# Kernel tuning notes

Measured on AMD Instinct MI355X. Metric: run time of the kernel, lower is better.

The kernel has to match this reference:

```python
import jax, jax.numpy as jnp
import numpy as np

B, S, D, H = 4, 1024, 2048, 16
HD = D // H
SCALE = float(np.sqrt(HD))


def setup_inputs() -> dict:
    key = jax.random.key(0)
    ks = jax.random.split(key, 11)
    std = 1.0 / np.sqrt(D)
    inp = {
        'q': jax.random.normal(ks[0], (B, S, D), jnp.float32),
        'k': jax.random.normal(ks[1], (B, S, D), jnp.float32),
        'v': jax.random.normal(ks[2], (B, S, D), jnp.float32),
        'wq_w': jax.random.uniform(ks[3], (D, D), jnp.float32, -std, std),
        'wq_b': jax.random.uniform(ks[4], (D,), jnp.float32, -std, std),
        'wk_w': jax.random.uniform(ks[5], (D, D), jnp.float32, -std, std),
        'wk_b': jax.random.uniform(ks[6], (D,), jnp.float32, -std, std),
        'wv_w': jax.random.uniform(ks[7], (D, D), jnp.float32, -std, std),
        'wv_b': jax.random.uniform(ks[8], (D,), jnp.float32, -std, std),
        'wo_w': jax.random.uniform(ks[9], (D, D), jnp.float32, -std, std),
        'wo_b': jax.random.uniform(ks[10], (D,), jnp.float32, -std, std),
    }
    return inp


def reference(q, k, v, wq_w, wq_b, wk_w, wk_b, wv_w, wv_b, wo_w, wo_b):
    # Linear projections (torch Linear: x @ W.T + b), split into heads: [B,H,S,HD]
    Q = (q @ wq_w.T + wq_b).reshape(B, S, H, HD).transpose(0, 2, 1, 3)
    K = (k @ wk_w.T + wk_b).reshape(B, S, H, HD).transpose(0, 2, 1, 3)
    V = (v @ wv_w.T + wv_b).reshape(B, S, H, HD).transpose(0, 2, 1, 3)
    # scaled dot-product attention; mask=None, dropout identity (eval)
    scores = jnp.einsum('bhqd,bhkd->bhqk', Q, K) / SCALE  # [B,H,S,S]
    attn = jax.nn.softmax(scores, axis=-1)
    context = jnp.einsum('bhqk,bhkd->bhqd', attn, V)      # [B,H,S,HD]
    context = context.transpose(0, 2, 1, 3).reshape(B, S, D)
    output = context @ wo_w.T + wo_b
    return output, attn
```

## Files before the change

kernel.cpp:

```cpp
#include <hip/hip_runtime.h>
#include <hip/hip_bf16.h>


typedef __attribute__((ext_vector_type(4)))  float f32x4;
typedef __attribute__((ext_vector_type(16))) float f32x16;
typedef __attribute__((ext_vector_type(8))) short  bf16x8;
typedef __attribute__((ext_vector_type(4))) short  short4v;
typedef __attribute__((ext_vector_type(8))) short  short8v;

__device__ __forceinline__ short f2b(float f) {
  __hip_bfloat16 h = __float2bfloat16(f);
  return __builtin_bit_cast(short, h);
}
__device__ __forceinline__ float b2f(short s) {
  __hip_bfloat16 h = __builtin_bit_cast(__hip_bfloat16, s);
  return __bfloat162float(h);
}

__global__ void cast_all(
    const float* __restrict__ q,  const float* __restrict__ k,  const float* __restrict__ v,
    const float* __restrict__ w0, const float* __restrict__ w1, const float* __restrict__ w2,
    const float* __restrict__ w3,
    __hip_bfloat16* __restrict__ qd, __hip_bfloat16* __restrict__ kd, __hip_bfloat16* __restrict__ vd,
    __hip_bfloat16* __restrict__ d0, __hip_bfloat16* __restrict__ d1, __hip_bfloat16* __restrict__ d2,
    __hip_bfloat16* __restrict__ d3)
{
  const int c0 = blockIdx.x * blockDim.x + threadIdx.x;
#pragma unroll
  for (int it = 0; it < 10; ++it) {
    int c = c0 + it * 524288;
    const float* in; __hip_bfloat16* out; size_t off;
    if (c < 3145728) {
      int seg = c >> 20; off = (size_t)(c & 1048575) * 8;
      in  = seg == 0 ? q  : (seg == 1 ? k  : v);
      out = seg == 0 ? qd : (seg == 1 ? kd : vd);
    } else {
      int c2 = c - 3145728;
      int seg = c2 >> 19; off = (size_t)(c2 & 524287) * 8;
      in  = seg == 0 ? w0 : (seg == 1 ? w1 : (seg == 2 ? w2 : w3));
      out = seg == 0 ? d0 : (seg == 1 ? d1 : (seg == 2 ? d2 : d3));
    }
    float4 a = *(const float4*)(in + off);
    float4 b = *(const float4*)(in + off + 4);
    short8v o;
    o[0] = f2b(a.x); o[1] = f2b(a.y); o[2] = f2b(a.z); o[3] = f2b(a.w);
    o[4] = f2b(b.x); o[5] = f2b(b.y); o[6] = f2b(b.z); o[7] = f2b(b.w);
    *(short8v*)(out + off) = o;
  }
}

__device__ __forceinline__ void gload_lds16(const __hip_bfloat16* g, char* l) {
  __builtin_amdgcn_global_load_lds(
      (const __attribute__((address_space(1))) unsigned int*)g,
      (__attribute__((address_space(3))) unsigned int*)l, 16, 0, 0);
}

template<bool SWAP>
__device__ __forceinline__ void gemm_core(
    const __hip_bfloat16* ga0, const __hip_bfloat16* gb0,
    char* As, char* Bs, char* lA0, char* lB0,
    int wm, int wn, int l16, int g, f32x4 (&acc)[4][4])
{
#pragma unroll 1
  for (int kt = 0; kt < 64; ++kt) {
    __syncthreads();
    gload_lds16(ga0,             lA0);
    gload_lds16(ga0 + 16 * 2048, lA0 + 1024);
    gload_lds16(gb0,             lB0);
    gload_lds16(gb0 + 16 * 2048, lB0 + 1024);
    ga0 += 32; gb0 += 32;
    asm volatile("s_waitcnt vmcnt(0)" ::: "memory");
    __syncthreads();
    bf16x8 a[4], b[4];
#pragma unroll
    for (int mf = 0; mf < 4; ++mf)
      a[mf] = *(const bf16x8*)(As + (wm + mf * 16 + l16) * 64 + g * 16);
#pragma unroll
    for (int nf = 0; nf < 4; ++nf)
      b[nf] = *(const bf16x8*)(Bs + (wn + nf * 16 + l16) * 64 + g * 16);
#pragma unroll
    for (int mf = 0; mf < 4; ++mf)
#pragma unroll
      for (int nf = 0; nf < 4; ++nf) {
        if (SWAP)
          acc[mf][nf] = __builtin_amdgcn_mfma_f32_16x16x32_bf16(b[nf], a[mf], acc[mf][nf], 0, 0, 0);
        else
          acc[mf][nf] = __builtin_amdgcn_mfma_f32_16x16x32_bf16(a[mf], b[nf], acc[mf][nf], 0, 0, 0);
      }
  }
}

__global__ __launch_bounds__(256, 2) void gemm_qkv(
    const __hip_bfloat16* __restrict__ qbf, const __hip_bfloat16* __restrict__ kbf,
    const __hip_bfloat16* __restrict__ vbf,
    const __hip_bfloat16* __restrict__ wqb, const __hip_bfloat16* __restrict__ wkb,
    const __hip_bfloat16* __restrict__ wvb,
    const float* __restrict__ bq, const float* __restrict__ bk, const float* __restrict__ bv,
    __hip_bfloat16* __restrict__ Qh, __hip_bfloat16* __restrict__ Kh,
    __hip_bfloat16* __restrict__ Vt)
{
  __shared__ __align__(16) char smem[34816];
  char* As = smem;
  char* Bs = smem + 16384;

  const int z = blockIdx.z;
  const __hip_bfloat16* A  = z == 0 ? qbf : (z == 1 ? kbf : vbf);
  const __hip_bfloat16* Bt = z == 0 ? wqb : (z == 1 ? wkb : wvb);
  const float* bias        = z == 0 ? bq  : (z == 1 ? bk  : bv);
  __hip_bfloat16* C        = z == 0 ? Qh  : (z == 1 ? Kh  : Vt);

  const int tid  = threadIdx.x;
  const int lane = tid & 63, wid = tid >> 6;
  const int l16  = lane & 15, g = lane >> 4;
  const int m0 = blockIdx.y * 128, n0 = blockIdx.x * 128;
  const int wm = (wid >> 1) * 64, wn = (wid & 1) * 64;

  f32x4 acc[4][4];
#pragma unroll
  for (int i = 0; i < 4; ++i)
#pragma unroll
    for (int j = 0; j < 4; ++j) acc[i][j] = f32x4{0.f, 0.f, 0.f, 0.f};

  const __hip_bfloat16* ga0 = A  + (size_t)(m0 + wid * 32 + (lane >> 2)) * 2048 + (lane & 3) * 8;
  const __hip_bfloat16* gb0 = Bt + (size_t)(n0 + wid * 32 + (lane >> 2)) * 2048 + (lane & 3) * 8;
  char* lA0 = As + wid * 2048;
  char* lB0 = Bs + wid * 2048;

  if (z == 2) gemm_core<false>(ga0, gb0, As, Bs, lA0, lB0, wm, wn, l16, g, acc);
  else        gemm_core<true >(ga0, gb0, As, Bs, lA0, lB0, wm, wn, l16, g, acc);

  const int h = n0 >> 7, bb = m0 >> 10, sbase = m0 & 1023;
  const int c8 = (tid & 15) * 8;
  __syncthreads();
  char* Cs = smem;
  if (z != 2) {
#pragma unroll
    for (int nf = 0; nf < 4; ++nf) {
      f32x4 bvv = *(const f32x4*)(bias + n0 + wn + nf * 16 + g * 4);
#pragma unroll
      for (int mf = 0; mf < 4; ++mf) {
        int m  = wm + mf * 16 + l16;
        int nc = wn + nf * 16 + g * 4;
        short4v pk;
#pragma unroll
        for (int r = 0; r < 4; ++r) pk[r] = f2b(acc[mf][nf][r] + bvv[r]);
        *(short4v*)(Cs + m * 272 + nc * 2) = pk;
      }
    }
    __syncthreads();
#pragma unroll
    for (int p = 0; p < 8; ++p) {
      int row = p * 16 + (tid >> 4);
      bf16x8 val = *(const bf16x8*)(Cs + row * 272 + c8 * 2);
      *(bf16x8*)(C + (((size_t)bb * 16 + h) * 1024 + sbase + row) * 128 + c8) = val;
    }
  } else {
#pragma unroll
    for (int nf = 0; nf < 4; ++nf) {
      float bvv = bias[n0 + wn + nf * 16 + l16];
#pragma unroll
      for (int mf = 0; mf < 4; ++mf) {
        int hd = wn + nf * 16 + l16;
        int s0 = wm + mf * 16 + g * 4;
        short4v pk;
#pragma unroll
        for (int r = 0; r < 4; ++r) pk[r] = f2b(acc[mf][nf][r] + bvv);
        *(short4v*)(Cs + hd * 272 + s0 * 2) = pk;
      }
    }
    __syncthreads();
#pragma unroll
    for (int p = 0; p < 8; ++p) {
      int hd = p * 16 + (tid >> 4);
      bf16x8 val = *(const bf16x8*)(Cs + hd * 272 + c8 * 2);
      *(bf16x8*)(C + (((size_t)bb * 16 + h) * 128 + hd) * 1024 + sbase + c8) = val;
    }
  }
}

__global__ __launch_bounds__(256, 2) void gemm_out(
    const __hip_bfloat16* __restrict__ A, const __hip_bfloat16* __restrict__ Bt,
    const float* __restrict__ bias, float* __restrict__ C)
{
  __shared__ __align__(16) char smem[32768];
  char* As = smem;
  char* Bs = smem + 16384;
  const int tid  = threadIdx.x;
  const int lane = tid & 63, wid = tid >> 6;
  const int l16  = lane & 15, g = lane >> 4;
  const int m0 = blockIdx.y * 128, n0 = blockIdx.x * 128;
  const int wm = (wid >> 1) * 64, wn = (wid & 1) * 64;

  f32x4 acc[4][4];
#pragma unroll
  for (int i = 0; i < 4; ++i)
#pragma unroll
    for (int j = 0; j < 4; ++j) acc[i][j] = f32x4{0.f, 0.f, 0.f, 0.f};

  const __hip_bfloat16* ga0 = A  + (size_t)(m0 + wid * 32 + (lane >> 2)) * 2048 + (lane & 3) * 8;
  const __hip_bfloat16* gb0 = Bt + (size_t)(n0 + wid * 32 + (lane >> 2)) * 2048 + (lane & 3) * 8;
  char* lA0 = As + wid * 2048;
  char* lB0 = Bs + wid * 2048;

  gemm_core<true>(ga0, gb0, As, Bs, lA0, lB0, wm, wn, l16, g, acc);

#pragma unroll
  for (int nf = 0; nf < 4; ++nf) {
    f32x4 bv = *(const f32x4*)(bias + n0 + wn + nf * 16 + g * 4);
#pragma unroll
    for (int mf = 0; mf < 4; ++mf) {
      int m = m0 + wm + mf * 16 + l16;
      int n = n0 + wn + nf * 16 + g * 4;
      f32x4 o;
#pragma unroll
      for (int r = 0; r < 4; ++r) o[r] = acc[mf][nf][r] + bv[r];
      *(f32x4*)(C + (size_t)m * 2048 + n) = o;
    }
  }
}

__global__ __launch_bounds__(512, 4) void attn_kernel(
    const __hip_bfloat16* __restrict__ Qh,
    const __hip_bfloat16* __restrict__ Kh,
    const __hip_bfloat16* __restrict__ Vt,
    float* __restrict__ attn,
    __hip_bfloat16* __restrict__ ctx)
{
  __shared__ __align__(16) char Plds[32 * 2048];
  __shared__ float red[8 * 32];
  __shared__ float invs[32];

  const int tid = threadIdx.x, lane = tid & 63, w = tid >> 6;
  const int l16 = lane & 15, g = lane >> 4;
  const int l31 = lane & 31, kh = lane >> 5;

  const int bid = blockIdx.x;
  const int xcd = bid & 7, j = bid >> 3;
  const int bh  = xcd * 8 + (j >> 5);
  const int q0  = (j & 31) << 5;

  const __hip_bfloat16* Qp = Qh + ((size_t)bh * 1024 + q0) * 128;
  const __hip_bfloat16* Kp = Kh + (size_t)bh * 1024 * 128;
  const __hip_bfloat16* Vp = Vt + (size_t)bh * 128 * 1024;
  float* ap = attn + ((size_t)bh * 1024 + q0) * 1024;

  bf16x8 qb[8];
#pragma unroll
  for (int s = 0; s < 8; ++s)
    qb[s] = *(const bf16x8*)(Qp + (size_t)l31 * 128 + s * 16 + kh * 8);

  const float esc = 0.08838834764831845f;
  float rs = 0.f;

#pragma unroll
  for (int pass = 0; pass < 4; ++pass) {
    const int keybase = pass * 256 + w * 32;
    const __hip_bfloat16* kr = Kp + (size_t)(keybase + l31) * 128 + kh * 8;
    bf16x8 kb[8];
#pragma unroll
    for (int s = 0; s < 8; ++s) kb[s] = *(const bf16x8*)(kr + s * 16);
    f32x16 acc;
#pragma unroll
    for (int i = 0; i < 16; ++i) acc[i] = 0.f;
    __builtin_amdgcn_s_setprio(1);
#pragma unroll
    for (int s = 0; s < 8; ++s)
      acc = __builtin_amdgcn_mfma_f32_32x32x16_bf16(kb[s], qb[s], acc, 0, 0, 0);
    __builtin_amdgcn_s_setprio(0);
#pragma unroll
    for (int grp = 0; grp < 4; ++grp) {
      short4v pk;
#pragma unroll
      for (int jj = 0; jj < 4; ++jj) {
        float e = __expf(acc[grp * 4 + jj] * esc);
        rs += e;
        pk[jj] = f2b(e);
      }
      int key0 = keybase + grp * 8 + kh * 4;
      *(short4v*)(Plds + l31 * 2048 + ((key0 * 2) ^ ((l31 & 7) << 4))) = pk;
    }
  }
  rs += __shfl_xor(rs, 32, 64);
  if (lane < 32) red[w * 32 + l31] = rs;
  __syncthreads();
  if (tid < 32) {
    float t = 0.f;
#pragma unroll
    for (int ww = 0; ww < 8; ++ww) t += red[ww * 32 + tid];
    invs[tid] = 1.0f / t;
  }

  f32x4 acc2[2];
  acc2[0] = f32x4{0.f, 0.f, 0.f, 0.f};
  acc2[1] = f32x4{0.f, 0.f, 0.f, 0.f};
  {
    const char* pr0 = Plds + l16 * 2048;
    const char* pr1 = Plds + (16 + l16) * 2048;
    const int sw = (l16 & 7) << 4;
#pragma unroll 4
    for (int kt = 0; kt < 32; ++kt) {
      int cb = (kt * 64 + g * 16) ^ sw;
      bf16x8 pa0 = *(const bf16x8*)(pr0 + cb);
      bf16x8 pa1 = *(const bf16x8*)(pr1 + cb);
      const __hip_bfloat16* vr = Vp + (size_t)(16 * w + l16) * 1024 + kt * 32 + g * 8;
      bf16x8 vb = *(const bf16x8*)vr;
      __builtin_amdgcn_s_setprio(1);
      acc2[0] = __builtin_amdgcn_mfma_f32_16x16x32_bf16(pa0, vb, acc2[0], 0, 0, 0);
      acc2[1] = __builtin_amdgcn_mfma_f32_16x16x32_bf16(pa1, vb, acc2[1], 0, 0, 0);
      __builtin_amdgcn_s_setprio(0);
    }
  }
  __syncthreads();

  {
    const int row = 4 * w + g;
    const float invr = invs[row];
    const char* rp = Plds + row * 2048;
    const int sw = (row & 7) << 4;
    float* apr = ap + (size_t)row * 1024;
#pragma unroll
    for (int it = 0; it < 16; ++it) {
      int col = it * 64 + l16 * 4;
      short4v pb = *(const short4v*)(rp + ((col * 2) ^ sw));
      f32x4 val;
#pragma unroll
      for (int r = 0; r < 4; ++r) val[r] = b2f(pb[r]) * invr;
      __builtin_nontemporal_store(val, (f32x4*)(apr + col));
    }
  }
  __syncthreads();

  {
    __hip_bfloat16* cs = (__hip_bfloat16*)Plds;
#pragma unroll
    for (int t = 0; t < 2; ++t) {
      f32x4 iv = *(const f32x4*)(invs + t * 16 + g * 4);
#pragma unroll
      for (int r = 0; r < 4; ++r)
        cs[(t * 16 + g * 4 + r) * 128 + 16 * w + l16] = __float2bfloat16(acc2[t][r] * iv[r]);
    }
    __syncthreads();
    const int row = tid >> 4, c8 = (tid & 15) * 8;
    bf16x8 val = *(const bf16x8*)(cs + row * 128 + c8);
    const int bb = bh >> 4, h = bh & 15;
    *(bf16x8*)(ctx + ((size_t)(bb * 1024 + q0 + row)) * 2048 + h * 128 + c8) = val;
  }
}

extern "C" void kernel_launch(void* const* d_in, const int* in_sizes, int n_in,
                              void* d_out, int out_size, void* d_ws, size_t ws_size,
                              hipStream_t stream) {
  const float* q    = (const float*)d_in[0];
  const float* k    = (const float*)d_in[1];
  const float* v    = (const float*)d_in[2];
  const float* wq_w = (const float*)d_in[3];
  const float* wq_b = (const float*)d_in[4];
  const float* wk_w = (const float*)d_in[5];
  const float* wk_b = (const float*)d_in[6];
  const float* wv_w = (const float*)d_in[7];
  const float* wv_b = (const float*)d_in[8];
  const float* wo_w = (const float*)d_in[9];
  const float* wo_b = (const float*)d_in[10];

  const size_t BSD = (size_t)4 * 1024 * 2048;
  const size_t DD  = (size_t)2048 * 2048;

  float* out  = (float*)d_out;
  float* attn = out + BSD;

  __hip_bfloat16* qbf = (__hip_bfloat16*)attn;
  __hip_bfloat16* kbf = qbf + BSD;
  __hip_bfloat16* vbf = kbf + BSD;

  __hip_bfloat16* wqb = (__hip_bfloat16*)d_ws;
  __hip_bfloat16* wkb = wqb + DD;
  __hip_bfloat16* wvb = wkb + DD;
  __hip_bfloat16* wob = wvb + DD;
  __hip_bfloat16* Qh  = wob + DD;
  __hip_bfloat16* Kh  = Qh + BSD;
  __hip_bfloat16* Vt  = Kh + BSD;
  __hip_bfloat16* ctx = Vt + BSD;

  cast_all<<<2048, 256, 0, stream>>>(q, k, v, wq_w, wk_w, wv_w, wo_w,
                                     qbf, kbf, vbf, wqb, wkb, wvb, wob);

  gemm_qkv<<<dim3(16, 32, 3), dim3(256), 0, stream>>>(
      qbf, kbf, vbf, wqb, wkb, wvb, wq_b, wk_b, wv_b, Qh, Kh, Vt);

  attn_kernel<<<dim3(2048), dim3(512), 0, stream>>>(Qh, Kh, Vt, attn, ctx);

  gemm_out<<<dim3(16, 32), dim3(256), 0, stream>>>(ctx, wob, wo_b, out);
}
```

Baseline: 372.3 us.

## Double GEMM K-step to 64 with XOR-swizzled LDS and raise occupancy

```diff
diff --git a/kernel.cpp b/kernel.cpp
--- a/kernel.cpp
+++ b/kernel.cpp
@@ -56,41 +56,51 @@
 }
 
 template<bool SWAP>
-__device__ __forceinline__ void gemm_core(
+__device__ __forceinline__ void gemm_core64(
     const __hip_bfloat16* ga0, const __hip_bfloat16* gb0,
     char* As, char* Bs, char* lA0, char* lB0,
     int wm, int wn, int l16, int g, f32x4 (&acc)[4][4])
 {
+  const int sw = (l16 & 7) << 4;
 #pragma unroll 1
-  for (int kt = 0; kt < 64; ++kt) {
+  for (int kt = 0; kt < 32; ++kt) {
     __syncthreads();
-    gload_lds16(ga0,             lA0);
-    gload_lds16(ga0 + 16 * 2048, lA0 + 1024);
-    gload_lds16(gb0,             lB0);
-    gload_lds16(gb0 + 16 * 2048, lB0 + 1024);
-    ga0 += 32; gb0 += 32;
+#pragma unroll
+    for (int c = 0; c < 4; ++c) {
+      gload_lds16(ga0 + c * 16384, lA0 + c * 1024);
+      gload_lds16(gb0 + c * 16384, lB0 + c * 1024);
+    }
+    ga0 += 64; gb0 += 64;
     asm volatile("s_waitcnt vmcnt(0)" ::: "memory");
     __syncthreads();
-    bf16x8 a[4], b[4];
-#pragma unroll
-    for (int mf = 0; mf < 4; ++mf)
-      a[mf] = *(const bf16x8*)(As + (wm + mf * 16 + l16) * 64 + g * 16);
-#pragma unroll
-    for (int nf = 0; nf < 4; ++nf)
-      b[nf] = *(const bf16x8*)(Bs + (wn + nf * 16 + l16) * 64 + g * 16);
-#pragma unroll
-    for (int mf = 0; mf < 4; ++mf)
+#pragma unroll
+    for (int ks = 0; ks < 2; ++ks) {
+      bf16x8 a[4];
+#pragma unroll
+      for (int mf = 0; mf < 4; ++mf)
+        a[mf] = *(const bf16x8*)(As + (wm + mf * 16 + l16) * 128 + ((ks * 64 + g * 16) ^ sw));
 #pragma unroll
       for (int nf = 0; nf < 4; ++nf) {
-        if (SWAP)
-          acc[mf][nf] = __builtin_amdgcn_mfma_f32_16x16x32_bf16(b[nf], a[mf], acc[mf][nf], 0, 0, 0);
-        else
-          acc[mf][nf] = __builtin_amdgcn_mfma_f32_16x16x32_bf16(a[mf], b[nf], acc[mf][nf], 0, 0, 0);
-      }
-  }
-}
-
-__global__ __launch_bounds__(256, 2) void gemm_qkv(
+        bf16x8 b = *(const bf16x8*)(Bs + (wn + nf * 16 + l16) * 128 + ((ks * 64 + g * 16) ^ sw));
+#pragma unroll
+        for (int mf = 0; mf < 4; ++mf) {
+          if (SWAP)
+            acc[mf][nf] = __builtin_amdgcn_mfma_f32_16x16x32_bf16(b, a[mf], acc[mf][nf], 0, 0, 0);
+          else
+            acc[mf][nf] = __builtin_amdgcn_mfma_f32_16x16x32_bf16(a[mf], b, acc[mf][nf], 0, 0, 0);
+        }
+      }
+    }
+  }
+}
+
+__device__ __forceinline__ const __hip_bfloat16* stage_src(
+    const __hip_bfloat16* M, int base, int wid, int lane) {
+  return M + (size_t)(base + wid * 32 + (lane >> 3)) * 2048
+           + (((lane & 7) ^ ((lane >> 3) & 7)) * 8);
+}
+
+__global__ __launch_bounds__(256, 3) void gemm_qkv(
     const __hip_bfloat16* __restrict__ qbf, const __hip_bfloat16* __restrict__ kbf,
     const __hip_bfloat16* __restrict__ vbf,
     const __hip_bfloat16* __restrict__ wqb, const __hip_bfloat16* __restrict__ wkb,
@@ -99,7 +109,7 @@
     __hip_bfloat16* __restrict__ Qh, __hip_bfloat16* __restrict__ Kh,
     __hip_bfloat16* __restrict__ Vt)
 {
-  __shared__ __align__(16) char smem[34816];
+  __shared__ __align__(16) char smem[32768];
   char* As = smem;
   char* Bs = smem + 16384;
 
@@ -121,64 +131,75 @@
 #pragma unroll
     for (int j = 0; j < 4; ++j) acc[i][j] = f32x4{0.f, 0.f, 0.f, 0.f};
 
-  const __hip_bfloat16* ga0 = A  + (size_t)(m0 + wid * 32 + (lane >> 2)) * 2048 + (lane & 3) * 8;
-  const __hip_bfloat16* gb0 = Bt + (size_t)(n0 + wid * 32 + (lane >> 2)) * 2048 + (lane & 3) * 8;
-  char* lA0 = As + wid * 2048;
-  char* lB0 = Bs + wid * 2048;
-
-  if (z == 2) gemm_core<false>(ga0, gb0, As, Bs, lA0, lB0, wm, wn, l16, g, acc);
-  else        gemm_core<true >(ga0, gb0, As, Bs, lA0, lB0, wm, wn, l16, g, acc);
-
-  const int h = n0 >> 7, bb = m0 >> 10, sbase = m0 & 1023;
+  const __hip_bfloat16* ga0 = stage_src(A,  m0, wid, lane);
+  const __hip_bfloat16* gb0 = stage_src(Bt, n0, wid, lane);
+  char* lA0 = As + wid * 4096;
+  char* lB0 = Bs + wid * 4096;
+
+  if (z == 2) gemm_core64<false>(ga0, gb0, As, Bs, lA0, lB0, wm, wn, l16, g, acc);
+  else        gemm_core64<true >(ga0, gb0, As, Bs, lA0, lB0, wm, wn, l16, g, acc);
+
+  const int hh = n0 >> 7, bb = m0 >> 10, sbase = m0 & 1023;
   const int c8 = (tid & 15) * 8;
-  __syncthreads();
   char* Cs = smem;
   if (z != 2) {
 #pragma unroll
-    for (int nf = 0; nf < 4; ++nf) {
-      f32x4 bvv = *(const f32x4*)(bias + n0 + wn + nf * 16 + g * 4);
-#pragma unroll
-      for (int mf = 0; mf < 4; ++mf) {
-        int m  = wm + mf * 16 + l16;
-        int nc = wn + nf * 16 + g * 4;
-        short4v pk;
-#pragma unroll
-        for (int r = 0; r < 4; ++r) pk[r] = f2b(acc[mf][nf][r] + bvv[r]);
-        *(short4v*)(Cs + m * 272 + nc * 2) = pk;
-      }
-    }
-    __syncthreads();
-#pragma unroll
-    for (int p = 0; p < 8; ++p) {
-      int row = p * 16 + (tid >> 4);
-      bf16x8 val = *(const bf16x8*)(Cs + row * 272 + c8 * 2);
-      *(bf16x8*)(C + (((size_t)bb * 16 + h) * 1024 + sbase + row) * 128 + c8) = val;
+    for (int h = 0; h < 2; ++h) {
+      __syncthreads();
+      if ((wid >> 1) == h) {
+#pragma unroll
+        for (int nf = 0; nf < 4; ++nf) {
+          f32x4 bvv = *(const f32x4*)(bias + n0 + wn + nf * 16 + g * 4);
+#pragma unroll
+          for (int mf = 0; mf < 4; ++mf) {
+            int sl = mf * 16 + l16;
+            int hd = wn + nf * 16 + g * 4;
+            short4v pk;
+#pragma unroll
+            for (int r = 0; r < 4; ++r) pk[r] = f2b(acc[mf][nf][r] + bvv[r]);
+            *(short4v*)(Cs + sl * 272 + hd * 2) = pk;
+          }
+        }
+      }
+      __syncthreads();
+#pragma unroll
+      for (int p = 0; p < 4; ++p) {
+        int rl = p * 16 + (tid >> 4);
+        bf16x8 val = *(const bf16x8*)(Cs + rl * 272 + c8 * 2);
+        *(bf16x8*)(C + (((size_t)bb * 16 + hh) * 1024 + sbase + h * 64 + rl) * 128 + c8) = val;
+      }
     }
   } else {
 #pragma unroll
-    for (int nf = 0; nf < 4; ++nf) {
-      float bvv = bias[n0 + wn + nf * 16 + l16];
-#pragma unroll
-      for (int mf = 0; mf < 4; ++mf) {
-        int hd = wn + nf * 16 + l16;
-        int s0 = wm + mf * 16 + g * 4;
-        short4v pk;
-#pragma unroll
-        for (int r = 0; r < 4; ++r) pk[r] = f2b(acc[mf][nf][r] + bvv);
-        *(short4v*)(Cs + hd * 272 + s0 * 2) = pk;
-      }
-    }
-    __syncthreads();
-#pragma unroll
-    for (int p = 0; p < 8; ++p) {
-      int hd = p * 16 + (tid >> 4);
-      bf16x8 val = *(const bf16x8*)(Cs + hd * 272 + c8 * 2);
-      *(bf16x8*)(C + (((size_t)bb * 16 + h) * 128 + hd) * 1024 + sbase + c8) = val;
-    }
-  }
-}
-
-__global__ __launch_bounds__(256, 2) void gemm_out(
+    for (int h = 0; h < 2; ++h) {
+      __syncthreads();
+      if ((wid & 1) == h) {
+#pragma unroll
+        for (int nf = 0; nf < 4; ++nf) {
+          float bvv = bias[n0 + wn + nf * 16 + l16];
+#pragma unroll
+          for (int mf = 0; mf < 4; ++mf) {
+            int hdl = nf * 16 + l16;
+            int s0  = wm + mf * 16 + g * 4;
+            short4v pk;
+#pragma unroll
+            for (int r = 0; r < 4; ++r) pk[r] = f2b(acc[mf][nf][r] + bvv);
+            *(short4v*)(Cs + hdl * 272 + s0 * 2) = pk;
+          }
+        }
+      }
+      __syncthreads();
+#pragma unroll
+      for (int p = 0; p < 4; ++p) {
+        int rl = p * 16 + (tid >> 4);
+        bf16x8 val = *(const bf16x8*)(Cs + rl * 272 + c8 * 2);
+        *(bf16x8*)(C + (((size_t)bb * 16 + hh) * 128 + h * 64 + rl) * 1024 + sbase + c8) = val;
+      }
+    }
+  }
+}
+
+__global__ __launch_bounds__(256, 3) void gemm_out(
     const __hip_bfloat16* __restrict__ A, const __hip_bfloat16* __restrict__ Bt,
     const float* __restrict__ bias, float* __restrict__ C)
 {
@@ -197,12 +218,12 @@
 #pragma unroll
     for (int j = 0; j < 4; ++j) acc[i][j] = f32x4{0.f, 0.f, 0.f, 0.f};
 
-  const __hip_bfloat16* ga0 = A  + (size_t)(m0 + wid * 32 + (lane >> 2)) * 2048 + (lane & 3) * 8;
-  const __hip_bfloat16* gb0 = Bt + (size_t)(n0 + wid * 32 + (lane >> 2)) * 2048 + (lane & 3) * 8;
-  char* lA0 = As + wid * 2048;
-  char* lB0 = Bs + wid * 2048;
-
-  gemm_core<true>(ga0, gb0, As, Bs, lA0, lB0, wm, wn, l16, g, acc);
+  const __hip_bfloat16* ga0 = stage_src(A,  m0, wid, lane);
+  const __hip_bfloat16* gb0 = stage_src(Bt, n0, wid, lane);
+  char* lA0 = As + wid * 4096;
+  char* lB0 = Bs + wid * 4096;
+
+  gemm_core64<true>(ga0, gb0, As, Bs, lA0, lB0, wm, wn, l16, g, acc);
 
 #pragma unroll
   for (int nf = 0; nf < 4; ++nf) {
@@ -249,7 +270,7 @@
   for (int s = 0; s < 8; ++s)
     qb[s] = *(const bf16x8*)(Qp + (size_t)l31 * 128 + s * 16 + kh * 8);
 
-  const float esc = 0.08838834764831845f;
+  const float esc2 = 0.12751744f;
   float rs = 0.f;
 
 #pragma unroll
@@ -272,7 +293,7 @@
       short4v pk;
 #pragma unroll
       for (int jj = 0; jj < 4; ++jj) {
-        float e = __expf(acc[grp * 4 + jj] * esc);
+        float e = exp2f(acc[grp * 4 + jj] * esc2);
         rs += e;
         pk[jj] = f2b(e);
       }
```

New measurement: 344.0 us. 1.08x faster.
